# Performance work log

Measured on AMD Instinct MI355X. Metric: run time of the kernel, lower is better.

Reference implementation:

```python
import jax, jax.numpy as jnp
import numpy as np

# --- fixed module hyperparameters (from init_kwargs) ---
B, N, DIM = 1, 1024, 1024
HEADS, KV_HEADS, DH = 16, 4, 64
BS = 32                 # block_size
NUM_SEL = 8             # num_selected_blocks (< num blocks, so min() is NUM_SEL)
MEM = 1                 # num_compressed_mem_kv
W = N // BS             # num compress blocks (seq divisible by block -> no padding paths)
G = HEADS // KV_HEADS   # grouped queries per kv head
CDIM = BS * DH          # compress mlp input dim
HID = CDIM              # compress_mlp_expand_factor = 1.0
EPS = 1e-6


def setup_inputs() -> dict:
    key = jax.random.key(0)
    ks = jax.random.split(key, 12)
    s = 0.02
    f32 = jnp.float32
    return {
        "inp": jax.random.normal(ks[0], (B, N, DIM), f32),
        "g_norm": jnp.ones((DIM,), f32),                                   # RMSNorm weight
        "w_qkv": jax.random.normal(ks[1], (DIM, (HEADS + 2 * KV_HEADS) * DH), f32) * s,
        "mem_kv": jax.random.normal(ks[2], (2, KV_HEADS, MEM, DH), f32) * s,
        "k_pos": jax.random.normal(ks[3], (KV_HEADS, BS, DH), f32) * s,    # intra-block pos
        "v_pos": jax.random.normal(ks[4], (KV_HEADS, BS, DH), f32) * s,
        "k_w1": jax.random.normal(ks[5], (CDIM, HID), f32) * s,
        "k_b1": jnp.zeros((HID,), f32),
        "k_w2": jax.random.normal(ks[6], (HID, DH), f32) * s,
        "k_b2": jnp.zeros((DH,), f32),
        "v_w1": jax.random.normal(ks[7], (CDIM, HID), f32) * s,
        "v_b1": jnp.zeros((HID,), f32),
        "v_w2": jax.random.normal(ks[8], (HID, DH), f32) * s,
        "v_b2": jnp.zeros((DH,), f32),
        "gate_w": jax.random.normal(ks[9], (DIM, 2 * HEADS), f32) * s,
        "gate_b": jnp.full((2 * HEADS,), -2.0, f32),                       # bias init from source
        "w_out": jax.random.normal(ks[10], (HEADS * DH, DIM), f32) * s,
    }


def _rotary(x):
    # interleaved rotary (rotary-embedding-torch default), x: (b, h, n, d)
    n, d = x.shape[-2], x.shape[-1]
    inv_freq = 1.0 / (10000.0 ** (jnp.arange(0, d, 2, dtype=jnp.float32) / d))
    freqs = jnp.arange(n, dtype=jnp.float32)[:, None] * inv_freq            # (n, d/2)
    cos = jnp.repeat(jnp.cos(freqs), 2, axis=-1).astype(x.dtype)
    sin = jnp.repeat(jnp.sin(freqs), 2, axis=-1).astype(x.dtype)
    xr = jnp.stack([-x[..., 1::2], x[..., 0::2]], axis=-1).reshape(x.shape)  # rotate_half
    return x * cos + xr * sin


def reference(inp, g_norm, w_qkv, mem_kv, k_pos, v_pos,
              k_w1, k_b1, k_w2, k_b2, v_w1, v_b1, v_w2, v_b2,
              gate_w, gate_b, w_out):
    scale = DH ** -0.5
    # RMSNorm
    x = inp * jax.lax.rsqrt(jnp.mean(jnp.square(inp), -1, keepdims=True) + EPS) * g_norm
    qkv = x @ w_qkv
    q = qkv[..., : HEADS * DH].reshape(B, N, HEADS, DH).transpose(0, 2, 1, 3)
    k = qkv[..., HEADS * DH : (HEADS + KV_HEADS) * DH].reshape(B, N, KV_HEADS, DH).transpose(0, 2, 1, 3)
    v = qkv[..., (HEADS + KV_HEADS) * DH :].reshape(B, N, KV_HEADS, DH).transpose(0, 2, 1, 3)

    # --- compressed branch: MLP-pool each block of BS keys/values ---
    kpe = k + jnp.tile(k_pos, (1, W, 1))[None]               # (B,KV,N,DH)
    vpe = v + jnp.tile(v_pos, (1, W, 1))[None]
    ck = jax.nn.relu(kpe.reshape(B, KV_HEADS, W, CDIM) @ k_w1 + k_b1) @ k_w2 + k_b2   # (B,KV,W,DH)
    cv = jax.nn.relu(vpe.reshape(B, KV_HEADS, W, CDIM) @ v_w1 + v_b1) @ v_w2 + v_b2
    ck = jnp.concatenate([jnp.broadcast_to(mem_kv[0], (B, KV_HEADS, MEM, DH)), ck], axis=2)
    cv = jnp.concatenate([jnp.broadcast_to(mem_kv[1], (B, KV_HEADS, MEM, DH)), cv], axis=2)

    qg = q.reshape(B, KV_HEADS, G, N, DH)
    csim = jnp.einsum('bhgid,bhjd->bhgij', qg, ck) * scale   # (B,KV,G,N,MEM+W)
    cattn = jax.nn.softmax(csim, axis=-1)
    c_out = jnp.einsum('bhgij,bhjd->bhgid', cattn, cv).reshape(B, HEADS, N, DH)

    # rotary only for the fine branch (applied after compressed attention)
    q = _rotary(q)
    k = _rotary(k)

    # --- block selection from compressed similarities (query heads share) ---
    imp = csim[..., MEM:].mean(axis=2)                       # (B,KV,N,W)
    imp = jnp.pad(imp, ((0, 0), (0, 0), (0, 0), (1, 0)), constant_values=-1000.0)
    imp = jax.nn.softmax(imp, axis=-1)[..., 1:]
    sel_vals, sel_idx = jax.lax.top_k(imp, NUM_SEL)          # (B,KV,N,S)
    fmask = sel_vals > 1e-10

    # always include each query's own block (diagonal block), fully attended
    own = jnp.broadcast_to((jnp.arange(N) // BS)[None, None, :, None], (B, KV_HEADS, N, 1))
    sel_idx = jnp.concatenate([sel_idx, own], axis=-1)       # (B,KV,N,S+1)
    fmask = jnp.concatenate([fmask, jnp.ones(own.shape, bool)], axis=-1)

    # --- gather selected KV blocks per query position (irregular access) ---
    kb = k.reshape(B, KV_HEADS, W, BS, DH)
    vb = v.reshape(B, KV_HEADS, W, BS, DH)
    b_ix = jnp.arange(B)[:, None, None, None]
    h_ix = jnp.arange(KV_HEADS)[None, :, None, None]
    J = (NUM_SEL + 1) * BS
    fk = kb[b_ix, h_ix, sel_idx].reshape(B, KV_HEADS, N, J, DH)
    fv = vb[b_ix, h_ix, sel_idx].reshape(B, KV_HEADS, N, J, DH)
    fmask = jnp.repeat(fmask, BS, axis=-1)                   # (B,KV,N,J)

    fq = q.reshape(B, KV_HEADS, G, N, DH)
    fsim = jnp.einsum('bhgid,bhijd->bhgij', fq, fk) * scale  # (B,KV,G,N,J)
    fsim = jnp.where(fmask[:, :, None], fsim, -jnp.finfo(fsim.dtype).max)
    fattn = jax.nn.softmax(fsim, axis=-1)
    f_out = jnp.einsum('bhgij,bhijd->bhgid', fattn, fv).reshape(B, HEADS, N, DH)

    # --- learned sigmoid gating of the two branches ---
    gates = jax.nn.sigmoid(x @ gate_w + gate_b).reshape(B, N, HEADS, 2).transpose(0, 2, 1, 3)
    out = gates[..., 0:1] * c_out + gates[..., 1:2] * f_out  # (B,H,N,DH)
    out = out.transpose(0, 2, 1, 3).reshape(B, N, HEADS * DH)
    return out @ w_out
```

## Files before the change

kernel.cpp:

```cpp
#include <hip/hip_runtime.h>
#include <math.h>

#define NTOK 1024
#define DDIM 1024
#define HEADS 16
#define KVH 4
#define DH 64
#define BSZ 32
#define NSEL 8
#define WBLK 32
#define GQ 4
#define CDIM 2048
#define HIDN 2048
#define QKVD 1536
#define SCALE 0.125f
#define NEGINF (-__builtin_inff())

typedef unsigned short u16;
typedef u16   u16x8  __attribute__((ext_vector_type(8)));
typedef short short8 __attribute__((ext_vector_type(8)));
typedef float f32x4  __attribute__((ext_vector_type(4)));

__device__ __forceinline__ u16 f2bf(float f) {
    unsigned u = __float_as_uint(f);
    return (u16)((u + 0x7fffu + ((u >> 16) & 1u)) >> 16);
}
__device__ __forceinline__ float bf2f(u16 h) { return __uint_as_float(((unsigned)h) << 16); }

__device__ __forceinline__ void glds16(const void* g, void* l) {
    __builtin_amdgcn_global_load_lds(
        (const __attribute__((address_space(1))) unsigned int*)g,
        (__attribute__((address_space(3))) unsigned int*)l, 16, 0, 0);
}

__device__ __forceinline__ size_t tiled_off(int row, int k, int K) {
    return ((size_t)((row >> 4) * (K >> 5) + (k >> 5)) * 64 +
            ((row & 15) | (((k >> 3) & 3) << 4))) * 8;
}

__device__ __forceinline__ void transpose_body(const float* __restrict__ W,
                                               u16* __restrict__ Thi, u16* __restrict__ Tlo,
                                               int K, int N, int bx, int by,
                                               float (*tile)[65]) {
    int k0 = by * 64, n0 = bx * 64;
    int t = threadIdx.x;
    int r = t >> 4, c4 = (t & 15) * 4;
#pragma unroll
    for (int p = 0; p < 4; ++p) {
        float4 v = *(const float4*)&W[(size_t)(k0 + r + p * 16) * N + n0 + c4];
        tile[r + p * 16][c4 + 0] = v.x;
        tile[r + p * 16][c4 + 1] = v.y;
        tile[r + p * 16][c4 + 2] = v.z;
        tile[r + p * 16][c4 + 3] = v.w;
    }
    __syncthreads();
    int n = t >> 2, ks = (t & 3) * 16;
#pragma unroll
    for (int c = 0; c < 2; ++c) {
        u16x8 h, l;
#pragma unroll
        for (int j = 0; j < 8; ++j) {
            float v = tile[ks + c * 8 + j][n];
            u16 hh = f2bf(v);
            h[j] = hh;
            l[j] = f2bf(v - bf2f(hh));
        }
        size_t ob = tiled_off(n0 + n, k0 + ks + c * 8, K);
        *(u16x8*)&Thi[ob] = h;
        if (Tlo) *(u16x8*)&Tlo[ob] = l;
    }
}

__device__ __forceinline__ void pad_body(const float* __restrict__ W, const float* __restrict__ b,
                                         u16* __restrict__ Thi, u16* __restrict__ Tlo,
                                         float* __restrict__ bias_pad, int K, int Xn, int KLOG,
                                         int bx) {
    int idx = bx * 256 + threadIdx.x;
    int k = (idx & ((K >> 3) - 1)) * 8;
    int n = idx >> (KLOG - 3);
    if (n >= 128) return;
    u16x8 h, l;
#pragma unroll
    for (int j = 0; j < 8; ++j) {
        float v = (n < Xn) ? W[(size_t)(k + j) * Xn + n] : 0.f;
        u16 hh = f2bf(v);
        h[j] = hh;
        l[j] = f2bf(v - bf2f(hh));
    }
    size_t ob = tiled_off(n, k, K);
    *(u16x8*)&Thi[ob] = h;
    *(u16x8*)&Tlo[ob] = l;
    if (k == 0) bias_pad[n] = (n < Xn) ? b[n] : 0.f;
}

__device__ __forceinline__ void rms_body(const float* __restrict__ inp, const float* __restrict__ g,
                                         u16* __restrict__ xhi, u16* __restrict__ xlo,
                                         int bx, float* red) {
    int t = threadIdx.x;
    int half = t >> 7, tid = t & 127;
    int n = bx * 2 + half;
    const float4* row = (const float4*)(inp + (size_t)n * DDIM);
    float4 v0 = row[tid * 2], v1 = row[tid * 2 + 1];
    float ss = v0.x*v0.x + v0.y*v0.y + v0.z*v0.z + v0.w*v0.w
             + v1.x*v1.x + v1.y*v1.y + v1.z*v1.z + v1.w*v1.w;
    for (int off = 32; off; off >>= 1) ss += __shfl_down(ss, off);
    if ((t & 63) == 0) red[t >> 6] = ss;
    __syncthreads();
    float tot = red[half * 2] + red[half * 2 + 1];
    float r = 1.f / sqrtf(tot * (1.f / DDIM) + 1e-6f);
    const float4* gp = (const float4*)g;
    float4 g0 = gp[tid * 2], g1 = gp[tid * 2 + 1];
    float o[8] = { v0.x*r*g0.x, v0.y*r*g0.y, v0.z*r*g0.z, v0.w*r*g0.w,
                   v1.x*r*g1.x, v1.y*r*g1.y, v1.z*r*g1.z, v1.w*r*g1.w };
    u16x8 h, l;
#pragma unroll
    for (int i = 0; i < 8; ++i) {
        u16 hh = f2bf(o[i]);
        h[i] = hh;
        l[i] = f2bf(o[i] - bf2f(hh));
    }
    size_t ob = tiled_off(n, tid * 8, DDIM);
    *(u16x8*)&xhi[ob] = h;
    *(u16x8*)&xlo[ob] = l;
}

__global__ void prep_kernel(const float* __restrict__ w_qkv, const float* __restrict__ k_w1,
                            const float* __restrict__ v_w1, const float* __restrict__ w_out,
                            const float* __restrict__ gate_w, const float* __restrict__ gate_b,
                            const float* __restrict__ k_w2, const float* __restrict__ k_b2,
                            const float* __restrict__ v_w2, const float* __restrict__ v_b2,
                            const float* __restrict__ inp, const float* __restrict__ g_norm,
                            u16* wqThi, u16* wqTlo, u16* kw1Thi, u16* kw1Tlo,
                            u16* vw1Thi, u16* vw1Tlo, u16* woThi,
                            u16* gwThi, u16* gwTlo, float* gbp,
                            u16* kw2Thi, u16* kw2Tlo, float* kb2p,
                            u16* vw2Thi, u16* vw2Tlo, float* vb2p,
                            u16* xhi, u16* xlo) {
    __shared__ float tile[64][65];
    __shared__ float red[4];
    int b = blockIdx.x;
    if (b < 384) {
        transpose_body(w_qkv, wqThi, wqTlo, DDIM, QKVD, b % 24, b / 24, tile);
    } else if (b < 1408) {
        int r = b - 384;
        transpose_body(k_w1, kw1Thi, kw1Tlo, CDIM, HIDN, r & 31, r >> 5, tile);
    } else if (b < 2432) {
        int r = b - 1408;
        transpose_body(v_w1, vw1Thi, vw1Tlo, CDIM, HIDN, r & 31, r >> 5, tile);
    } else if (b < 2688) {
        int r = b - 2432;
        transpose_body(w_out, woThi, nullptr, DDIM, DDIM, r & 15, r >> 4, tile);
    } else if (b < 2752) {
        pad_body(gate_w, gate_b, gwThi, gwTlo, gbp, DDIM, 32, 10, b - 2688);
    } else if (b < 2880) {
        pad_body(k_w2, k_b2, kw2Thi, kw2Tlo, kb2p, HIDN, 64, 11, b - 2752);
    } else if (b < 3008) {
        pad_body(v_w2, v_b2, vw2Thi, vw2Tlo, vb2p, HIDN, 64, 11, b - 2880);
    } else {
        rms_body(inp, g_norm, xhi, xlo, b - 3008, red);
    }
}

template<int SPLIT, int ACT, int FINAL>
__global__ __launch_bounds__(256, 1)
void gemm_tiled(const u16* __restrict__ Ahi0, const u16* __restrict__ Alo0,
                const u16* __restrict__ Bhi0, const u16* __restrict__ Blo0,
                const float* __restrict__ bias0, float* __restrict__ C0,
                const u16* __restrict__ Ahi1, const u16* __restrict__ Alo1,
                const u16* __restrict__ Bhi1, const u16* __restrict__ Blo1,
                const float* __restrict__ bias1, float* __restrict__ C1,
                int M, int N, int K, int S) {
    int batch = blockIdx.z / S;
    int s = blockIdx.z - batch * S;
    const u16* Ahi = batch ? Ahi1 : Ahi0;
    const u16* Alo = batch ? Alo1 : Alo0;
    const u16* Bhi = batch ? Bhi1 : Bhi0;
    const u16* Blo = batch ? Blo1 : Blo0;
    const float* bias = batch ? bias1 : bias0;
    float* C = batch ? C1 : C0;

    constexpr int PARTS = (SPLIT == 3) ? 2 : 1;
    __shared__ u16 smA[2 * PARTS * 8 * 512];
    __shared__ u16 smB[2 * PARTS * 8 * 512];

    int tid = threadIdx.x;
    int w = tid >> 6, L = tid & 63;
    int m15 = L & 15, q = L >> 4;
    int KT = K >> 5;
    int rowTile = blockIdx.y * 8, colTile = blockIdx.x * 8;
    int NIT = (K / S) >> 5;
    int kb0 = s * NIT;
    int aw = w & 1, bw = w >> 1;

    f32x4 acc[4][4];
#pragma unroll
    for (int i = 0; i < 4; ++i)
#pragma unroll
        for (int j = 0; j < 4; ++j) acc[i][j] = (f32x4){0.f, 0.f, 0.f, 0.f};

    auto stage = [&](int buf, int kb) {
#pragma unroll
        for (int rl = 0; rl < 2; ++rl) {
            int rb = 2 * w + rl;
            glds16(Ahi + ((size_t)(rowTile + rb) * KT + kb) * 512 + (size_t)L * 8,
                   &smA[((buf * PARTS + 0) * 8 + rb) * 512]);
            glds16(Bhi + ((size_t)(colTile + rb) * KT + kb) * 512 + (size_t)L * 8,
                   &smB[((buf * PARTS + 0) * 8 + rb) * 512]);
            if constexpr (SPLIT == 3) {
                glds16(Alo + ((size_t)(rowTile + rb) * KT + kb) * 512 + (size_t)L * 8,
                       &smA[((buf * PARTS + 1) * 8 + rb) * 512]);
                glds16(Blo + ((size_t)(colTile + rb) * KT + kb) * 512 + (size_t)L * 8,
                       &smB[((buf * PARTS + 1) * 8 + rb) * 512]);
            }
        }
    };

    stage(0, kb0);
    for (int it = 0; it < NIT; ++it) {
        __syncthreads();
        if (it + 1 < NIT) stage((it + 1) & 1, kb0 + it + 1);
        int buf = it & 1;
        short8 ah[4], bh[4];
#pragma unroll
        for (int i = 0; i < 4; ++i) {
            ah[i] = *(const short8*)&smA[((buf * PARTS + 0) * 8 + aw * 4 + i) * 512 + L * 8];
            bh[i] = *(const short8*)&smB[((buf * PARTS + 0) * 8 + bw * 4 + i) * 512 + L * 8];
        }
        if constexpr (SPLIT == 3) {
            short8 al[4], bl[4];
#pragma unroll
            for (int i = 0; i < 4; ++i) {
                al[i] = *(const short8*)&smA[((buf * PARTS + 1) * 8 + aw * 4 + i) * 512 + L * 8];
                bl[i] = *(const short8*)&smB[((buf * PARTS + 1) * 8 + bw * 4 + i) * 512 + L * 8];
            }
#pragma unroll
            for (int i = 0; i < 4; ++i)
#pragma unroll
                for (int j = 0; j < 4; ++j) {
                    acc[i][j] = __builtin_amdgcn_mfma_f32_16x16x32_bf16(ah[i], bl[j], acc[i][j], 0, 0, 0);
                    acc[i][j] = __builtin_amdgcn_mfma_f32_16x16x32_bf16(al[i], bh[j], acc[i][j], 0, 0, 0);
                    acc[i][j] = __builtin_amdgcn_mfma_f32_16x16x32_bf16(ah[i], bh[j], acc[i][j], 0, 0, 0);
                }
        } else {
#pragma unroll
            for (int i = 0; i < 4; ++i)
#pragma unroll
                for (int j = 0; j < 4; ++j)
                    acc[i][j] = __builtin_amdgcn_mfma_f32_16x16x32_bf16(ah[i], bh[j], acc[i][j], 0, 0, 0);
        }
    }

    if constexpr (FINAL == 0) C += (size_t)s * M * N;
#pragma unroll
    for (int i = 0; i < 4; ++i) {
        int row = rowTile * 16 + aw * 64 + i * 16 + q * 4;
#pragma unroll
        for (int j = 0; j < 4; ++j) {
            int col = colTile * 16 + bw * 64 + j * 16 + m15;
            float bv = (FINAL && bias) ? bias[col] : 0.f;
#pragma unroll
            for (int r = 0; r < 4; ++r) {
                float v = acc[i][j][r];
                if constexpr (FINAL) {
                    v += bv;
                    if (ACT == 1) v = fmaxf(v, 0.f);
                    if (ACT == 2) v = 1.f / (1.f + expf(-v));
                }
                C[(size_t)(row + r) * N + col] = v;
            }
        }
    }
}

template<int ACT>
__global__ void reduce_f32(const float* __restrict__ P0, const float* __restrict__ bias0,
                           float* __restrict__ C0,
                           const float* __restrict__ P1, const float* __restrict__ bias1,
                           float* __restrict__ C1, int S, int M, int N) {
    const float* P = blockIdx.y ? P1 : P0;
    const float* bias = blockIdx.y ? bias1 : bias0;
    float* C = blockIdx.y ? C1 : C0;
    int idx = blockIdx.x * 256 + threadIdx.x;
    int mn4 = (M * N) >> 2;
    if (idx >= mn4) return;
    f32x4 a = ((const f32x4*)P)[idx];
    for (int s = 1; s < S; ++s) a += ((const f32x4*)P)[(size_t)s * mn4 + idx];
    int col = (idx % (N >> 2)) * 4;
    f32x4 o;
#pragma unroll
    for (int j = 0; j < 4; ++j) {
        float v = a[j] + (bias ? bias[col + j] : 0.f);
        if (ACT == 1) v = fmaxf(v, 0.f);
        if (ACT == 2) v = 1.f / (1.f + expf(-v));
        o[j] = v;
    }
    ((f32x4*)C)[idx] = o;
}

__global__ void reduce_hid(const float* __restrict__ P0, const float* __restrict__ b0,
                           u16* __restrict__ hi0, u16* __restrict__ lo0,
                           const float* __restrict__ P1, const float* __restrict__ b1,
                           u16* __restrict__ hi1, u16* __restrict__ lo1, int S) {
    const float* P = blockIdx.y ? P1 : P0;
    const float* bias = blockIdx.y ? b1 : b0;
    u16* hi = blockIdx.y ? hi1 : hi0;
    u16* lo = blockIdx.y ? lo1 : lo0;
    int idx = blockIdx.x * 256 + threadIdx.x;
    int col = (idx & 255) * 8, rowi = idx >> 8;
    size_t base = ((size_t)rowi * HIDN + col) >> 2;
    f32x4 a0 = ((const f32x4*)P)[base], a1 = ((const f32x4*)P)[base + 1];
    for (int s = 1; s < S; ++s) {
        size_t sb = (size_t)s * (128 * HIDN / 4) + base;
        a0 += ((const f32x4*)P)[sb];
        a1 += ((const f32x4*)P)[sb + 1];
    }
    u16x8 h, l;
#pragma unroll
    for (int j = 0; j < 8; ++j) {
        float v = (j < 4 ? a0[j] : a1[j - 4]) + bias[col + j];
        v = fmaxf(v, 0.f);
        u16 hh = f2bf(v);
        h[j] = hh;
        l[j] = f2bf(v - bf2f(hh));
    }
    size_t ob = tiled_off(rowi, col, HIDN);
    *(u16x8*)&hi[ob] = h;
    *(u16x8*)&lo[ob] = l;
}

__global__ void reduce_ckcv(const float* __restrict__ Pk, const float* __restrict__ Pv,
                            const float* __restrict__ mem_kv,
                            const float* __restrict__ kb2, const float* __restrict__ vb2,
                            float* __restrict__ ck, float* __restrict__ cv, int S) {
    int idx = blockIdx.x * 256 + threadIdx.x;
    if (idx >= KVH * 33 * DH) return;
    int d = idx & 63;
    int j = (idx >> 6) % 33;
    int h = idx / (33 * 64);
    float kvv, vvv;
    if (j == 0) {
        kvv = mem_kv[(0 * KVH + h) * DH + d];
        vvv = mem_kv[(1 * KVH + h) * DH + d];
    } else {
        size_t base = (size_t)(h * WBLK + (j - 1)) * 128 + d;
        float ak = Pk[base], av = Pv[base];
        for (int s = 1; s < S; ++s) {
            ak += Pk[(size_t)s * (128 * 128) + base];
            av += Pv[(size_t)s * (128 * 128) + base];
        }
        kvv = ak + kb2[d];
        vvv = av + vb2[d];
    }
    ck[idx] = kvv;
    cv[idx] = vvv;
}

__global__ void build_cmlp_in(const float* __restrict__ qkv, const float* __restrict__ k_pos,
                              const float* __restrict__ v_pos,
                              u16* __restrict__ ckhi, u16* __restrict__ cklo,
                              u16* __restrict__ cvhi, u16* __restrict__ cvlo) {
    int idx = blockIdx.x * 256 + threadIdx.x;
    int k = (idx & 255) * 8;
    int r = idx >> 8;
    int p = k >> 6, d = k & 63;
    int h = r >> 5, wb = r & 31;
    int nn = wb * BSZ + p;
    const float* kq = qkv + (size_t)nn * QKVD + (HEADS + h) * DH + d;
    const float* vq = qkv + (size_t)nn * QKVD + (HEADS + KVH + h) * DH + d;
    const float* kp = k_pos + (size_t)(h * BSZ + p) * DH + d;
    const float* vp = v_pos + (size_t)(h * BSZ + p) * DH + d;
    u16x8 kh, kl, vh, vl;
#pragma unroll
    for (int j = 0; j < 8; ++j) {
        float kv = kq[j] + kp[j];
        float vv = vq[j] + vp[j];
        u16 a = f2bf(kv), b = f2bf(vv);
        kh[j] = a; kl[j] = f2bf(kv - bf2f(a));
        vh[j] = b; vl[j] = f2bf(vv - bf2f(b));
    }
    size_t ob = tiled_off(r, k, CDIM);
    *(u16x8*)&ckhi[ob] = kh; *(u16x8*)&cklo[ob] = kl;
    *(u16x8*)&cvhi[ob] = vh; *(u16x8*)&cvlo[ob] = vl;
}

__global__ void rotary_kernel(const float* __restrict__ qkv,
                              float* __restrict__ qr, float* __restrict__ kr,
                              float* __restrict__ vr) {
    int idx = blockIdx.x * 256 + threadIdx.x;
    int i = idx & 31;
    int n = (idx >> 5) & 1023;
    int hd = idx >> 15;
    if (hd >= 24) return;
    if (hd >= HEADS + KVH) {
        int h = hd - (HEADS + KVH);
        const float* src = qkv + (size_t)n * QKVD + (HEADS + KVH + h) * DH;
        float* dst = vr + ((size_t)h * NTOK + n) * DH;
        *(float2*)&dst[2 * i] = *(const float2*)&src[2 * i];
        return;
    }
    float inv = __expf((float)i * -0.28782313662425572f);
    float fr = (float)n * inv;
    float s, c;
    __sincosf(fr, &s, &c);
    const float* src; float* dst;
    if (hd < HEADS) { src = qkv + (size_t)n * QKVD + hd * DH;          dst = qr + ((size_t)hd * NTOK + n) * DH; }
    else { int h = hd - HEADS;
           src = qkv + (size_t)n * QKVD + (HEADS + h) * DH;            dst = kr + ((size_t)h * NTOK + n) * DH; }
    float2 x = *(const float2*)&src[2 * i];
    float2 o;
    o.x = x.x * c - x.y * s;
    o.y = x.y * c + x.x * s;
    *(float2*)&dst[2 * i] = o;
}

__global__ __launch_bounds__(256)
void cattn_kernel(const float* __restrict__ qkv, const float* __restrict__ ck,
                  const float* __restrict__ cv, float* __restrict__ c_out,
                  int* __restrict__ sel, int* __restrict__ selmask) {
    int h = blockIdx.y;
    int tid = threadIdx.x;
    int w = tid >> 6, lane = tid & 63;
    int grp = lane >> 4, sub = lane & 15;
    int n = blockIdx.x * 4 + w;
    __shared__ float cks[33 * 68];
    __shared__ float cvs[33 * 68];
    __shared__ float sims[16 * 36];

    for (int t4 = tid; t4 < 1056; t4 += 256) {
        int half = (t4 >= 528) ? 1 : 0;
        int u = t4 - half * 528;
        int j = u >> 4, d4 = (u & 15) * 4;
        const float* src = (half ? cv : ck) + (size_t)h * 33 * 64 + j * 64 + d4;
        float* dst = (half ? cvs : cks) + j * 68 + d4;
        *(float4*)dst = *(const float4*)src;
    }
    f32x4 qv[16];
    {
        const float4* qp4 = (const float4*)(qkv + (size_t)n * QKVD + (h * GQ + grp) * DH);
#pragma unroll
        for (int c = 0; c < 16; ++c) {
            float4 v = qp4[c];
            qv[c] = (f32x4){v.x, v.y, v.z, v.w};
        }
    }
    __syncthreads();

#pragma unroll
    for (int r = 0; r < 3; ++r) {
        int j = r * 16 + sub;
        if (j < 33) {
            f32x4 a0 = (f32x4){0.f, 0.f, 0.f, 0.f};
            f32x4 a1 = (f32x4){0.f, 0.f, 0.f, 0.f};
#pragma unroll
            for (int c = 0; c < 16; c += 2) {
                a0 += qv[c]     * (*(const f32x4*)&cks[j * 68 + c * 4]);
                a1 += qv[c + 1] * (*(const f32x4*)&cks[j * 68 + (c + 1) * 4]);
            }
            f32x4 at = a0 + a1;
            sims[(w * 4 + grp) * 36 + j] = ((at[0] + at[1]) + (at[2] + at[3])) * SCALE;
        }
    }

    float ival = NEGINF;
    if (lane < 32)
        ival = 0.25f * (sims[(w * 4 + 0) * 36 + 1 + lane] + sims[(w * 4 + 1) * 36 + 1 + lane] +
                        sims[(w * 4 + 2) * 36 + 1 + lane] + sims[(w * 4 + 3) * 36 + 1 + lane]);
    float m = ival;
    for (int off = 32; off; off >>= 1) m = fmaxf(m, __shfl_xor(m, off));
    float e = (lane < 32) ? expf(ival - m) : 0.f;
    float sum = e;
    for (int off = 32; off; off >>= 1) sum += __shfl_xor(sum, off);
    float p = (lane < 32) ? e / sum : NEGINF;

    float v = p;
    int base = (h * NTOK + n) * 9;
    for (int t = 0; t < NSEL; ++t) {
        float bv = v; int bi = lane;
        for (int off = 32; off; off >>= 1) {
            float ov = __shfl_xor(bv, off);
            int   oi = __shfl_xor(bi, off);
            if (ov > bv || (ov == bv && oi < bi)) { bv = ov; bi = oi; }
        }
        if (lane == 0) { sel[base + t] = bi; selmask[base + t] = (bv > 1e-10f) ? 1 : 0; }
        if (lane == bi) v = NEGINF;
    }
    if (lane == 0) { sel[base + NSEL] = n >> 5; selmask[base + NSEL] = 1; }

#pragma unroll
    for (int g = 0; g < 4; ++g) {
        float sv = (lane < 33) ? sims[(w * 4 + g) * 36 + lane] : NEGINF;
        float mm = sv;
        for (int off = 32; off; off >>= 1) mm = fmaxf(mm, __shfl_xor(mm, off));
        float ee = (lane < 33) ? __expf(sv - mm) : 0.f;
        float ssum = ee;
        for (int off = 32; off; off >>= 1) ssum += __shfl_xor(ssum, off);
        if (lane < 33) sims[(w * 4 + g) * 36 + lane] = ee / ssum;
    }

    f32x4 o = (f32x4){0.f, 0.f, 0.f, 0.f};
#pragma unroll
    for (int j = 0; j < 33; ++j) {
        float a = sims[(w * 4 + grp) * 36 + j];
        f32x4 vv = *(const f32x4*)&cvs[j * 68 + sub * 4];
        o += a * vv;
    }
    *(f32x4*)&c_out[(((size_t)(h * GQ + grp)) * NTOK + n) * DH + sub * 4] = o;
}

__global__ void fattn_kernel(const float* __restrict__ qr, const float* __restrict__ kr,
                             const float* __restrict__ vr, const int* __restrict__ sel,
                             const int* __restrict__ selmask, float* __restrict__ f_out) {
    int n = blockIdx.x, h = blockIdx.y;
    int tid = threadIdx.x;
    int w = tid >> 6, lane = tid & 63;
    int grp = lane >> 4, sub = lane & 15;
    __shared__ float qsm[4 * 68];
    __shared__ float Ksm[64 * 64];
    __shared__ float Vsm[64 * 64];
    __shared__ float ps[4 * 68];
    __shared__ float msm[16], lsm[16];
    __shared__ int sel_s[9], msk_s[9];

    if (tid < 9) {
        sel_s[tid] = sel[(h * NTOK + n) * 9 + tid];
        msk_s[tid] = selmask[(h * NTOK + n) * 9 + tid];
    }
    qsm[w * 68 + lane] = qr[(((size_t)(h * GQ + w)) * NTOK + n) * DH + lane];
    f32x4 o4 = (f32x4){0.f, 0.f, 0.f, 0.f};
    float m_run = -3.402823466e38f, l_run = 0.f;
    __syncthreads();

    const float* krh_ = kr + (size_t)h * NTOK * DH;
    const float* vrh_ = vr + (size_t)h * NTOK * DH;

    int rl = lane >> 4, sl = lane & 15;

    auto stageRows = [&](float* dstbuf, const float* src, int bp) {
        int nrow = (bp < 4) ? 64 : 32;
        if (w * 16 < nrow) {
            int myblk = sel_s[bp * 2 + (w >> 1)];
            const float* b_ = src + (size_t)myblk * BSZ * DH;
#pragma unroll
            for (int cc = 0; cc < 4; ++cc) {
                int r = w * 16 + cc * 4 + rl;
                int sg = sl ^ (r & 15);
                glds16(b_ + (size_t)(r & 31) * DH + sg * 4, &dstbuf[(w * 16 + cc * 4) * 64]);
            }
        }
    };

    stageRows(Ksm, krh_, 0);
    stageRows(Vsm, vrh_, 0);

    for (int bp = 0; bp < 5; ++bp) {
        int nrow = (bp < 4) ? 64 : 32;

        asm volatile("s_waitcnt vmcnt(4)" ::: "memory");
        __builtin_amdgcn_sched_barrier(0);

        float s = -3.402823466e38f;
        {
            int jj = w * 16 + sub;
            int b = bp * 2 + (jj >> 5);
            if (jj < nrow && msk_s[b]) {
                int sw = jj & 15;
                const float* Kb = &Ksm[jj * 64];
                f32x4 a0 = (f32x4){0.f, 0.f, 0.f, 0.f};
                f32x4 a1 = (f32x4){0.f, 0.f, 0.f, 0.f};
#pragma unroll
                for (int c = 0; c < 16; c += 2) {
                    f32x4 k4a = *(const f32x4*)&Kb[(c ^ sw) * 4];
                    f32x4 q4a = *(const f32x4*)&qsm[grp * 68 + c * 4];
                    f32x4 k4b = *(const f32x4*)&Kb[((c + 1) ^ sw) * 4];
                    f32x4 q4b = *(const f32x4*)&qsm[grp * 68 + (c + 1) * 4];
                    a0 += q4a * k4a;
                    a1 += q4b * k4b;
                }
                f32x4 at = a0 + a1;
                s = ((at[0] + at[1]) + (at[2] + at[3])) * SCALE;
            }
        }
        float mb = s;
        for (int off = 8; off; off >>= 1) mb = fmaxf(mb, __shfl_xor(mb, off));
        float m_new = fmaxf(m_run, mb);
        float pp = (s > -1e37f) ? __expf(s - m_new) : 0.f;
        float alpha = __expf(m_run - m_new);
        float psum = pp;
        for (int off = 8; off; off >>= 1) psum += __shfl_xor(psum, off);
        l_run = l_run * alpha + psum;
        m_run = m_new;
        ps[w * 68 + grp * 16 + sub] = pp;

        __builtin_amdgcn_sched_barrier(0);
        asm volatile("s_waitcnt lgkmcnt(0)" ::: "memory");
        __builtin_amdgcn_sched_barrier(0);
        if (bp < 4) {
            stageRows(Ksm, krh_, bp + 1);
            asm volatile("s_waitcnt vmcnt(4)" ::: "memory");
        } else {
            asm volatile("s_waitcnt vmcnt(0)" ::: "memory");
        }
        __builtin_amdgcn_sched_barrier(0);

        {
            f32x4 t0 = (f32x4){0.f, 0.f, 0.f, 0.f};
            f32x4 t1 = (f32x4){0.f, 0.f, 0.f, 0.f};
            int jbase = w * 16;
            if (jbase < nrow) {
#pragma unroll
                for (int jq = 0; jq < 4; ++jq) {
                    f32x4 p4 = *(const f32x4*)&ps[w * 68 + grp * 16 + jq * 4];
#pragma unroll
                    for (int r = 0; r < 4; ++r) {
                        int row = jbase + jq * 4 + r;
                        int slot = sub ^ (row & 15);
                        f32x4 vv = *(const f32x4*)&Vsm[row * 64 + slot * 4];
                        if (r & 1) t1 += p4[r] * vv;
                        else       t0 += p4[r] * vv;
                    }
                }
            }
            o4 = o4 * alpha + (t0 + t1);
        }
        if (bp < 4) {
            __builtin_amdgcn_sched_barrier(0);
            asm volatile("s_waitcnt lgkmcnt(0)" ::: "memory");
            __builtin_amdgcn_sched_barrier(0);
            stageRows(Vsm, vrh_, bp + 1);
        }
    }
    if (sub == 0) { msm[w * 4 + grp] = m_run; lsm[w * 4 + grp] = l_run; }
    __syncthreads();
    *(f32x4*)&Ksm[(w * 4 + grp) * 64 + sub * 4] = o4;
    __syncthreads();
    float m0 = msm[0 * 4 + w], m1 = msm[1 * 4 + w], m2 = msm[2 * 4 + w], m3 = msm[3 * 4 + w];
    float M = fmaxf(fmaxf(m0, m1), fmaxf(m2, m3));
    float f0 = __expf(m0 - M), f1 = __expf(m1 - M), f2 = __expf(m2 - M), f3 = __expf(m3 - M);
    float L = lsm[0 * 4 + w] * f0 + lsm[1 * 4 + w] * f1 + lsm[2 * 4 + w] * f2 + lsm[3 * 4 + w] * f3;
    float sum = Ksm[(0 * 4 + w) * 64 + lane] * f0 + Ksm[(1 * 4 + w) * 64 + lane] * f1
              + Ksm[(2 * 4 + w) * 64 + lane] * f2 + Ksm[(3 * 4 + w) * 64 + lane] * f3;
    f_out[(((size_t)(h * GQ + w)) * NTOK + n) * DH + lane] = sum / L;
}

__global__ void mix_kernel(const float* __restrict__ gates, const float* __restrict__ c_out,
                           const float* __restrict__ f_out,
                           u16* __restrict__ mixhi, u16* __restrict__ mixlo) {
    int idx = blockIdx.x * 256 + threadIdx.x;
    int col = (idx & 127) * 8;
    int n = idx >> 7;
    int hd = col >> 6, d = col & 63;
    float g0 = gates[(size_t)n * 128 + hd * 2];
    float g1 = gates[(size_t)n * 128 + hd * 2 + 1];
    size_t hoff = (((size_t)hd) * NTOK + n) * DH + d;
    u16x8 h, l;
#pragma unroll
    for (int j = 0; j < 8; ++j) {
        float v = g0 * c_out[hoff + j] + g1 * f_out[hoff + j];
        u16 hh = f2bf(v);
        h[j] = hh;
        l[j] = f2bf(v - bf2f(hh));
    }
    size_t ob = tiled_off(n, col, DDIM);
    *(u16x8*)&mixhi[ob] = h;
    *(u16x8*)&mixlo[ob] = l;
}

extern "C" void kernel_launch(void* const* d_in, const int* in_sizes, int n_in,
                              void* d_out, int out_size, void* d_ws, size_t ws_size,
                              hipStream_t stream) {
    const float* inp    = (const float*)d_in[0];
    const float* g_norm = (const float*)d_in[1];
    const float* w_qkv  = (const float*)d_in[2];
    const float* mem_kv = (const float*)d_in[3];
    const float* k_pos  = (const float*)d_in[4];
    const float* v_pos  = (const float*)d_in[5];
    const float* k_w1   = (const float*)d_in[6];
    const float* k_b1   = (const float*)d_in[7];
    const float* k_w2   = (const float*)d_in[8];
    const float* k_b2   = (const float*)d_in[9];
    const float* v_w1   = (const float*)d_in[10];
    const float* v_b1   = (const float*)d_in[11];
    const float* v_w2   = (const float*)d_in[12];
    const float* v_b2   = (const float*)d_in[13];
    const float* gate_w = (const float*)d_in[14];
    const float* gate_b = (const float*)d_in[15];
    const float* w_out  = (const float*)d_in[16];
    float* out = (float*)d_out;

    char* wsb = (char*)d_ws;
    size_t off = 0;
    auto alloc = [&](size_t bytes) -> void* {
        void* p = wsb + off;
        off = (off + bytes + 255) & ~(size_t)255;
        return p;
    };
    u16*   xhi    = (u16*)  alloc((size_t)NTOK * DDIM * 2);
    u16*   xlo    = (u16*)  alloc((size_t)NTOK * DDIM * 2);
    float* qkvb   = (float*)alloc((size_t)NTOK * QKVD * 4);
    u16*   wqThi  = (u16*)  alloc((size_t)QKVD * DDIM * 2);
    u16*   wqTlo  = (u16*)  alloc((size_t)QKVD * DDIM * 2);
    u16*   kw1Thi = (u16*)  alloc((size_t)HIDN * CDIM * 2);
    u16*   kw1Tlo = (u16*)  alloc((size_t)HIDN * CDIM * 2);
    u16*   vw1Thi = (u16*)  alloc((size_t)HIDN * CDIM * 2);
    u16*   vw1Tlo = (u16*)  alloc((size_t)HIDN * CDIM * 2);
    u16*   woThi  = (u16*)  alloc((size_t)DDIM * DDIM * 2);
    u16*   gwThi  = (u16*)  alloc((size_t)128 * DDIM * 2);
    u16*   gwTlo  = (u16*)  alloc((size_t)128 * DDIM * 2);
    float* gbp    = (float*)alloc(128 * 4);
    u16*   kw2Thi = (u16*)  alloc((size_t)128 * HIDN * 2);
    u16*   kw2Tlo = (u16*)  alloc((size_t)128 * HIDN * 2);
    float* kb2p   = (float*)alloc(128 * 4);
    u16*   vw2Thi = (u16*)  alloc((size_t)128 * HIDN * 2);
    u16*   vw2Tlo = (u16*)  alloc((size_t)128 * HIDN * 2);
    float* vb2p   = (float*)alloc(128 * 4);
    u16*   cinkhi = (u16*)  alloc((size_t)128 * CDIM * 2);
    u16*   cinklo = (u16*)  alloc((size_t)128 * CDIM * 2);
    u16*   cinvhi = (u16*)  alloc((size_t)128 * CDIM * 2);
    u16*   cinvlo = (u16*)  alloc((size_t)128 * CDIM * 2);
    u16*   hidkhi = (u16*)  alloc((size_t)128 * HIDN * 2);
    u16*   hidklo = (u16*)  alloc((size_t)128 * HIDN * 2);
    u16*   hidvhi = (u16*)  alloc((size_t)128 * HIDN * 2);
    u16*   hidvlo = (u16*)  alloc((size_t)128 * HIDN * 2);
    float* Pg     = (float*)alloc((size_t)8 * NTOK * 128 * 4);
    float* Pm1k   = (float*)alloc((size_t)4 * 128 * HIDN * 4);
    float* Pm1v   = (float*)alloc((size_t)4 * 128 * HIDN * 4);
    float* Pm2k   = (float*)alloc((size_t)8 * 128 * 128 * 4);
    float* Pm2v   = (float*)alloc((size_t)8 * 128 * 128 * 4);
    float* ck     = (float*)alloc((size_t)KVH * 33 * DH * 4);
    float* cv     = (float*)alloc((size_t)KVH * 33 * DH * 4);
    float* qr     = (float*)alloc((size_t)HEADS * NTOK * DH * 4);
    float* kr     = (float*)alloc((size_t)KVH * NTOK * DH * 4);
    float* vr     = (float*)alloc((size_t)KVH * NTOK * DH * 4);
    float* c_out  = (float*)alloc((size_t)HEADS * NTOK * DH * 4);
    float* f_out  = (float*)alloc((size_t)HEADS * NTOK * DH * 4);
    float* gates  = (float*)alloc((size_t)NTOK * 128 * 4);
    int*   sel    = (int*)  alloc((size_t)KVH * NTOK * 9 * 4);
    int*   selmask= (int*)  alloc((size_t)KVH * NTOK * 9 * 4);
    u16*   mixhi  = (u16*)  alloc((size_t)NTOK * DDIM * 2);
    u16*   mixlo  = (u16*)  alloc((size_t)NTOK * DDIM * 2);

    prep_kernel<<<3520, 256, 0, stream>>>(
        w_qkv, k_w1, v_w1, w_out, gate_w, gate_b, k_w2, k_b2, v_w2, v_b2,
        inp, g_norm,
        wqThi, wqTlo, kw1Thi, kw1Tlo, vw1Thi, vw1Tlo, woThi,
        gwThi, gwTlo, gbp, kw2Thi, kw2Tlo, kb2p, vw2Thi, vw2Tlo, vb2p,
        xhi, xlo);

    gemm_tiled<3, 0, 1><<<dim3(QKVD / 128, NTOK / 128, 1), 256, 0, stream>>>(
        xhi, xlo, wqThi, wqTlo, nullptr, qkvb,
        xhi, xlo, wqThi, wqTlo, nullptr, qkvb, NTOK, QKVD, DDIM, 1);
    gemm_tiled<3, 0, 0><<<dim3(1, NTOK / 128, 8), 256, 0, stream>>>(
        xhi, xlo, gwThi, gwTlo, nullptr, Pg,
        xhi, xlo, gwThi, gwTlo, nullptr, Pg, NTOK, 128, DDIM, 8);
    reduce_f32<2><<<dim3(128, 1), 256, 0, stream>>>(Pg, gbp, gates, Pg, gbp, gates, 8, NTOK, 128);
    build_cmlp_in<<<128, 256, 0, stream>>>(qkvb, k_pos, v_pos, cinkhi, cinklo, cinvhi, cinvlo);
    gemm_tiled<3, 0, 0><<<dim3(HIDN / 128, 1, 8), 256, 0, stream>>>(
        cinkhi, cinklo, kw1Thi, kw1Tlo, nullptr, Pm1k,
        cinvhi, cinvlo, vw1Thi, vw1Tlo, nullptr, Pm1v, 128, HIDN, CDIM, 4);
    reduce_hid<<<dim3(128, 2), 256, 0, stream>>>(Pm1k, k_b1, hidkhi, hidklo,
                                                 Pm1v, v_b1, hidvhi, hidvlo, 4);
    gemm_tiled<3, 0, 0><<<dim3(1, 1, 16), 256, 0, stream>>>(
        hidkhi, hidklo, kw2Thi, kw2Tlo, nullptr, Pm2k,
        hidvhi, hidvlo, vw2Thi, vw2Tlo, nullptr, Pm2v, 128, 128, HIDN, 8);
    reduce_ckcv<<<33, 256, 0, stream>>>(Pm2k, Pm2v, mem_kv, kb2p, vb2p, ck, cv, 8);
    rotary_kernel<<<(24 * NTOK * 32) / 256, 256, 0, stream>>>(qkvb, qr, kr, vr);
    cattn_kernel<<<dim3(NTOK / 4, KVH), 256, 0, stream>>>(qkvb, ck, cv, c_out, sel, selmask);
    fattn_kernel<<<dim3(NTOK, KVH), 256, 0, stream>>>(qr, kr, vr, sel, selmask, f_out);
    mix_kernel<<<(NTOK * DDIM / 8) / 256, 256, 0, stream>>>(gates, c_out, f_out, mixhi, mixlo);
    gemm_tiled<1, 0, 1><<<dim3(DDIM / 128, NTOK / 128, 1), 256, 0, stream>>>(
        mixhi, mixhi, woThi, woThi, nullptr, out,
        mixhi, mixhi, woThi, woThi, nullptr, out, NTOK, DDIM, DDIM, 1);
}
```

Baseline: 330.0 us.

## Fuse gate projection into QKV GEMM and split-K the output projection

The gate weights are packed as extra padded columns of the QKV weight (1536→1664), so one GEMM produces qkv and gate logits together. This removes the separate gate GEMM and its reduce, and the sigmoid plus bias moves into the mix kernel. The output projection now runs split-K with 2 slices into a scratch buffer, followed by a reduce kernel. That doubles the grid for better CU utilization but adds an extra launch and partial-sum traffic.

```diff
diff --git a/kernel.cpp b/kernel.cpp
--- a/kernel.cpp
+++ b/kernel.cpp
@@ -13,8 +13,11 @@
 #define CDIM 2048
 #define HIDN 2048
 #define QKVD 1536
+#define QKVG 1664
 #define SCALE 0.125f
 #define NEGINF (-__builtin_inff())
+
+#define OFFGATE ((size_t)96 * 32 * 512)
 
 typedef unsigned short u16;
 typedef u16   u16x8  __attribute__((ext_vector_type(8)));
@@ -90,7 +93,7 @@
     size_t ob = tiled_off(n, k, K);
     *(u16x8*)&Thi[ob] = h;
     *(u16x8*)&Tlo[ob] = l;
-    if (k == 0) bias_pad[n] = (n < Xn) ? b[n] : 0.f;
+    if (bias_pad && k == 0) bias_pad[n] = (n < Xn) ? b[n] : 0.f;
 }
 
 __device__ __forceinline__ void rms_body(const float* __restrict__ inp, const float* __restrict__ g,
@@ -126,13 +129,12 @@
 
 __global__ void prep_kernel(const float* __restrict__ w_qkv, const float* __restrict__ k_w1,
                             const float* __restrict__ v_w1, const float* __restrict__ w_out,
-                            const float* __restrict__ gate_w, const float* __restrict__ gate_b,
+                            const float* __restrict__ gate_w,
                             const float* __restrict__ k_w2, const float* __restrict__ k_b2,
                             const float* __restrict__ v_w2, const float* __restrict__ v_b2,
                             const float* __restrict__ inp, const float* __restrict__ g_norm,
                             u16* wqThi, u16* wqTlo, u16* kw1Thi, u16* kw1Tlo,
                             u16* vw1Thi, u16* vw1Tlo, u16* woThi,
-                            u16* gwThi, u16* gwTlo, float* gbp,
                             u16* kw2Thi, u16* kw2Tlo, float* kb2p,
                             u16* vw2Thi, u16* vw2Tlo, float* vb2p,
                             u16* xhi, u16* xlo) {
@@ -151,7 +153,7 @@
         int r = b - 2432;
         transpose_body(w_out, woThi, nullptr, DDIM, DDIM, r & 15, r >> 4, tile);
     } else if (b < 2752) {
-        pad_body(gate_w, gate_b, gwThi, gwTlo, gbp, DDIM, 32, 10, b - 2688);
+        pad_body(gate_w, nullptr, wqThi + OFFGATE, wqTlo + OFFGATE, nullptr, DDIM, 32, 10, b - 2688);
     } else if (b < 2880) {
         pad_body(k_w2, k_b2, kw2Thi, kw2Tlo, kb2p, HIDN, 64, 11, b - 2752);
     } else if (b < 3008) {
@@ -365,8 +367,8 @@
     int p = k >> 6, d = k & 63;
     int h = r >> 5, wb = r & 31;
     int nn = wb * BSZ + p;
-    const float* kq = qkv + (size_t)nn * QKVD + (HEADS + h) * DH + d;
-    const float* vq = qkv + (size_t)nn * QKVD + (HEADS + KVH + h) * DH + d;
+    const float* kq = qkv + (size_t)nn * QKVG + (HEADS + h) * DH + d;
+    const float* vq = qkv + (size_t)nn * QKVG + (HEADS + KVH + h) * DH + d;
     const float* kp = k_pos + (size_t)(h * BSZ + p) * DH + d;
     const float* vp = v_pos + (size_t)(h * BSZ + p) * DH + d;
     u16x8 kh, kl, vh, vl;
@@ -393,7 +395,7 @@
     if (hd >= 24) return;
     if (hd >= HEADS + KVH) {
         int h = hd - (HEADS + KVH);
-        const float* src = qkv + (size_t)n * QKVD + (HEADS + KVH + h) * DH;
+        const float* src = qkv + (size_t)n * QKVG + (HEADS + KVH + h) * DH;
         float* dst = vr + ((size_t)h * NTOK + n) * DH;
         *(float2*)&dst[2 * i] = *(const float2*)&src[2 * i];
         return;
@@ -403,9 +405,9 @@
     float s, c;
     __sincosf(fr, &s, &c);
     const float* src; float* dst;
-    if (hd < HEADS) { src = qkv + (size_t)n * QKVD + hd * DH;          dst = qr + ((size_t)hd * NTOK + n) * DH; }
+    if (hd < HEADS) { src = qkv + (size_t)n * QKVG + hd * DH;          dst = qr + ((size_t)hd * NTOK + n) * DH; }
     else { int h = hd - HEADS;
-           src = qkv + (size_t)n * QKVD + (HEADS + h) * DH;            dst = kr + ((size_t)h * NTOK + n) * DH; }
+           src = qkv + (size_t)n * QKVG + (HEADS + h) * DH;            dst = kr + ((size_t)h * NTOK + n) * DH; }
     float2 x = *(const float2*)&src[2 * i];
     float2 o;
     o.x = x.x * c - x.y * s;
@@ -436,7 +438,7 @@
     }
     f32x4 qv[16];
     {
-        const float4* qp4 = (const float4*)(qkv + (size_t)n * QKVD + (h * GQ + grp) * DH);
+        const float4* qp4 = (const float4*)(qkv + (size_t)n * QKVG + (h * GQ + grp) * DH);
 #pragma unroll
         for (int c = 0; c < 16; ++c) {
             float4 v = qp4[c];
@@ -642,15 +644,17 @@
     f_out[(((size_t)(h * GQ + w)) * NTOK + n) * DH + lane] = sum / L;
 }
 
-__global__ void mix_kernel(const float* __restrict__ gates, const float* __restrict__ c_out,
-                           const float* __restrict__ f_out,
+__global__ void mix_kernel(const float* __restrict__ qkvg, const float* __restrict__ gate_b,
+                           const float* __restrict__ c_out, const float* __restrict__ f_out,
                            u16* __restrict__ mixhi, u16* __restrict__ mixlo) {
     int idx = blockIdx.x * 256 + threadIdx.x;
     int col = (idx & 127) * 8;
     int n = idx >> 7;
     int hd = col >> 6, d = col & 63;
-    float g0 = gates[(size_t)n * 128 + hd * 2];
-    float g1 = gates[(size_t)n * 128 + hd * 2 + 1];
+    float r0 = qkvg[(size_t)n * QKVG + QKVD + hd * 2]     + gate_b[hd * 2];
+    float r1 = qkvg[(size_t)n * QKVG + QKVD + hd * 2 + 1] + gate_b[hd * 2 + 1];
+    float g0 = 1.f / (1.f + expf(-r0));
+    float g1 = 1.f / (1.f + expf(-r1));
     size_t hoff = (((size_t)hd) * NTOK + n) * DH + d;
     u16x8 h, l;
 #pragma unroll
@@ -696,17 +700,14 @@
     };
     u16*   xhi    = (u16*)  alloc((size_t)NTOK * DDIM * 2);
     u16*   xlo    = (u16*)  alloc((size_t)NTOK * DDIM * 2);
-    float* qkvb   = (float*)alloc((size_t)NTOK * QKVD * 4);
-    u16*   wqThi  = (u16*)  alloc((size_t)QKVD * DDIM * 2);
-    u16*   wqTlo  = (u16*)  alloc((size_t)QKVD * DDIM * 2);
+    float* qkvg   = (float*)alloc((size_t)NTOK * QKVG * 4);
+    u16*   wqThi  = (u16*)  alloc((size_t)QKVG * DDIM * 2);
+    u16*   wqTlo  = (u16*)  alloc((size_t)QKVG * DDIM * 2);
     u16*   kw1Thi = (u16*)  alloc((size_t)HIDN * CDIM * 2);
     u16*   kw1Tlo = (u16*)  alloc((size_t)HIDN * CDIM * 2);
     u16*   vw1Thi = (u16*)  alloc((size_t)HIDN * CDIM * 2);
     u16*   vw1Tlo = (u16*)  alloc((size_t)HIDN * CDIM * 2);
     u16*   woThi  = (u16*)  alloc((size_t)DDIM * DDIM * 2);
-    u16*   gwThi  = (u16*)  alloc((size_t)128 * DDIM * 2);
-    u16*   gwTlo  = (u16*)  alloc((size_t)128 * DDIM * 2);
-    float* gbp    = (float*)alloc(128 * 4);
     u16*   kw2Thi = (u16*)  alloc((size_t)128 * HIDN * 2);
     u16*   kw2Tlo = (u16*)  alloc((size_t)128 * HIDN * 2);
     float* kb2p   = (float*)alloc(128 * 4);
@@ -721,7 +722,6 @@
     u16*   hidklo = (u16*)  alloc((size_t)128 * HIDN * 2);
     u16*   hidvhi = (u16*)  alloc((size_t)128 * HIDN * 2);
     u16*   hidvlo = (u16*)  alloc((size_t)128 * HIDN * 2);
-    float* Pg     = (float*)alloc((size_t)8 * NTOK * 128 * 4);
     float* Pm1k   = (float*)alloc((size_t)4 * 128 * HIDN * 4);
     float* Pm1v   = (float*)alloc((size_t)4 * 128 * HIDN * 4);
     float* Pm2k   = (float*)alloc((size_t)8 * 128 * 128 * 4);
@@ -733,27 +733,23 @@
     float* vr     = (float*)alloc((size_t)KVH * NTOK * DH * 4);
     float* c_out  = (float*)alloc((size_t)HEADS * NTOK * DH * 4);
     float* f_out  = (float*)alloc((size_t)HEADS * NTOK * DH * 4);
-    float* gates  = (float*)alloc((size_t)NTOK * 128 * 4);
     int*   sel    = (int*)  alloc((size_t)KVH * NTOK * 9 * 4);
     int*   selmask= (int*)  alloc((size_t)KVH * NTOK * 9 * 4);
     u16*   mixhi  = (u16*)  alloc((size_t)NTOK * DDIM * 2);
     u16*   mixlo  = (u16*)  alloc((size_t)NTOK * DDIM * 2);
+    float* Pout   = Pm1k;
 
     prep_kernel<<<3520, 256, 0, stream>>>(
-        w_qkv, k_w1, v_w1, w_out, gate_w, gate_b, k_w2, k_b2, v_w2, v_b2,
+        w_qkv, k_w1, v_w1, w_out, gate_w, k_w2, k_b2, v_w2, v_b2,
         inp, g_norm,
         wqThi, wqTlo, kw1Thi, kw1Tlo, vw1Thi, vw1Tlo, woThi,
-        gwThi, gwTlo, gbp, kw2Thi, kw2Tlo, kb2p, vw2Thi, vw2Tlo, vb2p,
+        kw2Thi, kw2Tlo, kb2p, vw2Thi, vw2Tlo, vb2p,
         xhi, xlo);
 
-    gemm_tiled<3, 0, 1><<<dim3(QKVD / 128, NTOK / 128, 1), 256, 0, stream>>>(
-        xhi, xlo, wqThi, wqTlo, nullptr, qkvb,
-        xhi, xlo, wqThi, wqTlo, nullptr, qkvb, NTOK, QKVD, DDIM, 1);
-    gemm_tiled<3, 0, 0><<<dim3(1, NTOK / 128, 8), 256, 0, stream>>>(
-        xhi, xlo, gwThi, gwTlo, nullptr, Pg,
-        xhi, xlo, gwThi, gwTlo, nullptr, Pg, NTOK, 128, DDIM, 8);
-    reduce_f32<2><<<dim3(128, 1), 256, 0, stream>>>(Pg, gbp, gates, Pg, gbp, gates, 8, NTOK, 128);
-    build_cmlp_in<<<128, 256, 0, stream>>>(qkvb, k_pos, v_pos, cinkhi, cinklo, cinvhi, cinvlo);
+    gemm_tiled<3, 0, 1><<<dim3(QKVG / 128, NTOK / 128, 1), 256, 0, stream>>>(
+        xhi, xlo, wqThi, wqTlo, nullptr, qkvg,
+        xhi, xlo, wqThi, wqTlo, nullptr, qkvg, NTOK, QKVG, DDIM, 1);
+    build_cmlp_in<<<128, 256, 0, stream>>>(qkvg, k_pos, v_pos, cinkhi, cinklo, cinvhi, cinvlo);
     gemm_tiled<3, 0, 0><<<dim3(HIDN / 128, 1, 8), 256, 0, stream>>>(
         cinkhi, cinklo, kw1Thi, kw1Tlo, nullptr, Pm1k,
         cinvhi, cinvlo, vw1Thi, vw1Tlo, nullptr, Pm1v, 128, HIDN, CDIM, 4);
@@ -763,11 +759,13 @@
         hidkhi, hidklo, kw2Thi, kw2Tlo, nullptr, Pm2k,
         hidvhi, hidvlo, vw2Thi, vw2Tlo, nullptr, Pm2v, 128, 128, HIDN, 8);
     reduce_ckcv<<<33, 256, 0, stream>>>(Pm2k, Pm2v, mem_kv, kb2p, vb2p, ck, cv, 8);
-    rotary_kernel<<<(24 * NTOK * 32) / 256, 256, 0, stream>>>(qkvb, qr, kr, vr);
-    cattn_kernel<<<dim3(NTOK / 4, KVH), 256, 0, stream>>>(qkvb, ck, cv, c_out, sel, selmask);
+    rotary_kernel<<<(24 * NTOK * 32) / 256, 256, 0, stream>>>(qkvg, qr, kr, vr);
+    cattn_kernel<<<dim3(NTOK / 4, KVH), 256, 0, stream>>>(qkvg, ck, cv, c_out, sel, selmask);
     fattn_kernel<<<dim3(NTOK, KVH), 256, 0, stream>>>(qr, kr, vr, sel, selmask, f_out);
-    mix_kernel<<<(NTOK * DDIM / 8) / 256, 256, 0, stream>>>(gates, c_out, f_out, mixhi, mixlo);
-    gemm_tiled<1, 0, 1><<<dim3(DDIM / 128, NTOK / 128, 1), 256, 0, stream>>>(
-        mixhi, mixhi, woThi, woThi, nullptr, out,
-        mixhi, mixhi, woThi, woThi, nullptr, out, NTOK, DDIM, DDIM, 1);
-}
+    mix_kernel<<<(NTOK * DDIM / 8) / 256, 256, 0, stream>>>(qkvg, gate_b, c_out, f_out, mixhi, mixlo);
+    gemm_tiled<1, 0, 0><<<dim3(DDIM / 128, NTOK / 128, 2), 256, 0, stream>>>(
+        mixhi, mixhi, woThi, woThi, nullptr, Pout,
+        mixhi, mixhi, woThi, woThi, nullptr, Pout, NTOK, DDIM, DDIM, 2);
+    reduce_f32<0><<<dim3((NTOK * DDIM / 4) / 256, 1), 256, 0, stream>>>(
+        Pout, nullptr, out, Pout, nullptr, out, 2, NTOK, DDIM);
+}
```

After: 308.8 us. -6.4%, faster.
